# Performance work log

Measured on AMD Instinct MI355X. Metric: run time of the kernel, lower is better.

The kernel has to match this reference:

```python
import jax, jax.numpy as jnp
import numpy as np

DIM = 768      # model dim
H = 12         # heads
HD = DIM // H  # head dim = 64
T = 8          # num_frames // 2 (video temporal frames)
SF = 8         # spec_frames (audio temporal frames)
AP = 196       # audio patches per frame
VP = 196       # video patches per frame
B = 4          # batch
SCALE = HD ** (-0.5)  # 0.125


def setup_inputs() -> dict:
    key = jax.random.key(0)
    ks = jax.random.split(key, 12)
    n = lambda k, shape, s=1.0: s * jax.random.normal(k, shape, dtype=jnp.float32)
    return {
        "s_x": n(ks[0], (2 + AP, B * SF, DIM)),
        "t_x": n(ks[1], (1 + VP, B * T, DIM)),
        "clip_space_pos": n(ks[2], (AP, DIM), SCALE),
        "vmae_space_pos": n(ks[3], (VP, DIM), SCALE),
        "clip_temporal_pos": n(ks[4], (SF, DIM), SCALE),
        "vmae_temporal_pos": n(ks[5], (T, DIM), SCALE),
        "q_w": n(ks[6], (DIM, DIM), 0.02),
        "q_b": jnp.zeros((DIM,), jnp.float32),
        "kv_w": n(ks[7], (2 * DIM, DIM), 0.02),
        "kv_b": jnp.zeros((2 * DIM,), jnp.float32),
        "proj_w": n(ks[8], (DIM, DIM), 0.02),
        "proj_b": jnp.zeros((DIM,), jnp.float32),
    }


def _prep(pat, space_pos, temp_pos, tt):
    # pat: (n, b*tt, d) ; rearrange 'n (b t) d -> b t n d', add space pos,
    # 'b t n d -> b n t d', add temporal pos, 'b n t d -> b (n t) d'
    n, bt, d = pat.shape
    b = bt // tt
    x = pat.reshape(n, b, tt, d).transpose(1, 2, 0, 3)      # b t n d
    x = x + space_pos                                        # (n,d) bcast
    x = x.transpose(0, 2, 1, 3) + temp_pos                   # b n t d + (t,d)
    return x.reshape(b, n * tt, d)


def reference(s_x, t_x, clip_space_pos, vmae_space_pos, clip_temporal_pos,
              vmae_temporal_pos, q_w, q_b, kv_w, kv_b, proj_w, proj_b):
    t_x_cls = t_x[:1]                                        # (1, b*T, d)
    s_pat = _prep(s_x[2:], clip_space_pos, clip_temporal_pos, SF)   # (b, AP*SF, d)
    t_pat = _prep(t_x[1:], vmae_space_pos, vmae_temporal_pos, T)    # (b, VP*T, d)

    b, N, d = t_pat.shape
    M = s_pat.shape[1]
    q = t_pat @ q_w.T + q_b                                  # (b, N, d)
    q = q.reshape(b, N, H, HD).transpose(0, 2, 1, 3)         # b h n hd
    kv = s_pat @ kv_w.T + kv_b                               # (b, M, 2d)
    kv = kv.reshape(b, M, 2, H, HD).transpose(2, 0, 3, 1, 4) # 2 b h m hd
    k, v = kv[0], kv[1]

    attn = jax.nn.softmax(jnp.einsum('bhnd,bhmd->bhnm', q * SCALE, k), axis=-1)
    out = jnp.einsum('bhnm,bhmd->bhnd', attn, v)             # b h n hd
    out = out.transpose(0, 2, 1, 3).reshape(b, N, d)         # b n d
    out = out @ proj_w.T + proj_b

    # 'b (n t) d -> n (b t) d'
    out = out.reshape(b, VP, T, d).transpose(1, 0, 2, 3).reshape(VP, b * T, d)
    return jnp.concatenate([t_x_cls, out], axis=0)           # (1+VP, b*T, d)
```

## Files before the change

kernel.cpp:

```cpp
#include <hip/hip_runtime.h>
#include <hip/hip_bf16.h>

#define DIM 768
#define NH 12
#define HD 64
#define NSEQ 1568
#define ROWS 6272
#define QSC2 0.18033688011112042f
#define RGN 100352

typedef __attribute__((ext_vector_type(8))) short short8;
typedef __attribute__((ext_vector_type(4))) float f32x4;
typedef __attribute__((ext_vector_type(4))) unsigned short u16x4;
typedef unsigned short ushort_t;
typedef unsigned int uint_t;

static __device__ __forceinline__ ushort_t f2bf(float f) {
    union { float f; uint_t u; } c; c.f = f;
    uint_t u = c.u + 0x7fffu + ((c.u >> 16) & 1u);
    return (ushort_t)(u >> 16);
}
static __device__ __forceinline__ int cvt_pk_bf16(float lo, float hi) {
    int r;
    asm("v_cvt_pk_bf16_f32 %0, %1, %2" : "=v"(r) : "v"(lo), "v"(hi));
    return r;
}
static __device__ __forceinline__ void glds16(const short* g, short* l) {
    __builtin_amdgcn_global_load_lds(
        (const __attribute__((address_space(1))) void*)g,
        (__attribute__((address_space(3))) void*)l, 16, 0, 0);
}

#define SM_HALF(S, PF, LR)                                                    \
    {                                                                         \
        float p_[4][4];                                                       \
        _Pragma("unroll")                                                     \
        for (int jb = 0; jb < 4; ++jb) {                                      \
            _Pragma("unroll")                                                 \
            for (int r = 0; r < 4; ++r)                                       \
                p_[jb][r] = __builtin_amdgcn_exp2f(S[jb][r]);                 \
        }                                                                     \
        float rs_ = ((p_[0][0] + p_[0][1]) + (p_[0][2] + p_[0][3]))           \
                  + ((p_[1][0] + p_[1][1]) + (p_[1][2] + p_[1][3]))           \
                  + ((p_[2][0] + p_[2][1]) + (p_[2][2] + p_[2][3]))           \
                  + ((p_[3][0] + p_[3][1]) + (p_[3][2] + p_[3][3]));          \
        rs_ += __shfl_xor(rs_, 16);                                           \
        rs_ += __shfl_xor(rs_, 32);                                           \
        LR += rs_;                                                            \
        int pw_[4][2];                                                        \
        _Pragma("unroll")                                                     \
        for (int jb = 0; jb < 4; ++jb) {                                      \
            pw_[jb][0] = cvt_pk_bf16(p_[jb][0], p_[jb][1]);                   \
            pw_[jb][1] = cvt_pk_bf16(p_[jb][2], p_[jb][3]);                   \
        }                                                                     \
        _Pragma("unroll")                                                     \
        for (int jb2 = 0; jb2 < 2; ++jb2) {                                   \
            int S0_ = gh ? pw_[jb2 * 2 + 1][0] : pw_[jb2 * 2][0];             \
            int S1_ = gh ? pw_[jb2 * 2 + 1][1] : pw_[jb2 * 2][1];             \
            union { int i[4]; short8 s; } fr_;                                \
            fr_.i[0] = __builtin_amdgcn_ds_bpermute(addr0, S0_);              \
            fr_.i[1] = __builtin_amdgcn_ds_bpermute(addr0, S1_);              \
            fr_.i[2] = __builtin_amdgcn_ds_bpermute(addr1, S0_);              \
            fr_.i[3] = __builtin_amdgcn_ds_bpermute(addr1, S1_);              \
            PF[jb2] = fr_.s;                                                  \
        }                                                                     \
    }

#define PREP_HALF (ROWS * (DIM / 8))
#define W8 (DIM * DIM / 8)
#define CLS4 (32 * DIM / 4)
__global__ __launch_bounds__(256)
void prep_all(const float* __restrict__ src_t, const float* __restrict__ src_s,
              const float* __restrict__ vsp, const float* __restrict__ csp,
              const float* __restrict__ vtp, const float* __restrict__ ctp,
              const float* __restrict__ qw, const float* __restrict__ kvw,
              const float* __restrict__ pw, const float* __restrict__ txc,
              short* __restrict__ dst_t, short* __restrict__ dst_s,
              short* __restrict__ dq, short* __restrict__ dkv,
              short* __restrict__ dp, float* __restrict__ out_cls) {
    int idx = blockIdx.x * 256 + threadIdx.x;
    if (idx < 2 * PREP_HALF) {
        int sel = idx >= PREP_HALF;
        int i0  = sel ? idx - PREP_HALF : idx;
        const float* src  = sel ? src_s : src_t;
        const float* spos = sel ? csp : vsp;
        const float* tpos = sel ? ctp : vtp;
        short* dst = sel ? dst_s : dst_t;
        int d8  = i0 % (DIM / 8);
        int row = i0 / (DIM / 8);
        int b = row / NSEQ;
        int i = row % NSEQ;
        int n = i >> 3;
        int t = i & 7;
        const float4* s4 = reinterpret_cast<const float4*>(src + ((size_t)n * 32 + b * 8 + t) * DIM + d8 * 8);
        const float4* p4 = reinterpret_cast<const float4*>(spos + (size_t)n * DIM + d8 * 8);
        const float4* q4 = reinterpret_cast<const float4*>(tpos + (size_t)t * DIM + d8 * 8);
        union { int w[4]; short8 v; } o;
        float4 a0 = s4[0], a1 = s4[1], b0 = p4[0], b1 = p4[1], c0 = q4[0], c1 = q4[1];
        o.w[0] = cvt_pk_bf16(a0.x + b0.x + c0.x, a0.y + b0.y + c0.y);
        o.w[1] = cvt_pk_bf16(a0.z + b0.z + c0.z, a0.w + b0.w + c0.w);
        o.w[2] = cvt_pk_bf16(a1.x + b1.x + c1.x, a1.y + b1.y + c1.y);
        o.w[3] = cvt_pk_bf16(a1.z + b1.z + c1.z, a1.w + b1.w + c1.w);
        reinterpret_cast<short8*>(dst)[i0] = o.v;
    } else if (idx < 2 * PREP_HALF + 4 * W8) {
        int i0 = idx - 2 * PREP_HALF;
        const float* src; short* dst; int off;
        if (i0 < W8)            { src = qw;  dst = dq;  off = i0; }
        else if (i0 < 3 * W8)   { src = kvw; dst = dkv; off = i0 - W8; }
        else                    { src = pw;  dst = dp;  off = i0 - 3 * W8; }
        const float4* s4 = reinterpret_cast<const float4*>(src + (size_t)off * 8);
        float4 a0 = s4[0], a1 = s4[1];
        union { int w[4]; short8 v; } o;
        o.w[0] = cvt_pk_bf16(a0.x, a0.y);
        o.w[1] = cvt_pk_bf16(a0.z, a0.w);
        o.w[2] = cvt_pk_bf16(a1.x, a1.y);
        o.w[3] = cvt_pk_bf16(a1.z, a1.w);
        reinterpret_cast<short8*>(dst)[off] = o.v;
    } else {
        int i0 = idx - (2 * PREP_HALF + 4 * W8);
        reinterpret_cast<float4*>(out_cls)[i0] = reinterpret_cast<const float4*>(txc)[i0];
    }
}

__global__ __launch_bounds__(256)
void gemm_qkv(const short* __restrict__ tpat, const short* __restrict__ spat,
              const short* __restrict__ wq, const short* __restrict__ wkv,
              const float* __restrict__ q_b, const float* __restrict__ kv_b,
              ushort_t* __restrict__ qout, ushort_t* __restrict__ kout,
              ushort_t* __restrict__ vtout) {
    __shared__ short As[2][128 * 32];
    __shared__ short Ws[2][128 * 32];
    const int t = threadIdx.x;
    const int l = t & 63, w = t >> 6;
    const int Li = l & 15, Lg = l >> 4;
    int orig = blockIdx.x;
    int xcd = orig & 7, idxq = orig >> 3;
    int wg = (xcd < 2 ? xcd * 111 : 222 + (xcd - 2) * 110) + idxq;
    const int x = wg % 18, y = wg / 18;
    const int mode = (x >= 6);
    const short* A  = mode ? spat : tpat;
    const short* Wm = mode ? wkv : wq;
    const float* bias = mode ? kv_b : q_b;
    const int c0 = (mode ? x - 6 : x) * 128;
    const int r0 = y * 128;
    const int wrow = (w >> 1) * 64, wcol = (w & 1) * 64;

    f32x4 acc[4][4];
    #pragma unroll
    for (int i = 0; i < 4; ++i)
        #pragma unroll
        for (int j = 0; j < 4; ++j) acc[i][j] = (f32x4){0.f, 0.f, 0.f, 0.f};

    const short* Ag = A  + (size_t)(r0 + w * 32 + (l >> 2)) * DIM + (l & 3) * 8;
    const short* Wg = Wm + (size_t)(c0 + w * 32 + (l >> 2)) * DIM + (l & 3) * 8;

    glds16(Ag,                    &As[0][(w * 32) * 32]);
    glds16(Ag + (size_t)16 * DIM, &As[0][(w * 32 + 16) * 32]);
    glds16(Wg,                    &Ws[0][(w * 32) * 32]);
    glds16(Wg + (size_t)16 * DIM, &Ws[0][(w * 32 + 16) * 32]);
    __syncthreads();

    int cur = 0;
    for (int k0 = 0; k0 < DIM; k0 += 32) {
        if (k0 + 32 < DIM) {
            int nb = cur ^ 1;
            glds16(Ag + k0 + 32,                    &As[nb][(w * 32) * 32]);
            glds16(Ag + (size_t)16 * DIM + k0 + 32, &As[nb][(w * 32 + 16) * 32]);
            glds16(Wg + k0 + 32,                    &Ws[nb][(w * 32) * 32]);
            glds16(Wg + (size_t)16 * DIM + k0 + 32, &Ws[nb][(w * 32 + 16) * 32]);
        }
        short8 af[4], wf[4];
        #pragma unroll
        for (int mi = 0; mi < 4; ++mi)
            af[mi] = *reinterpret_cast<const short8*>(&As[cur][(wrow + mi * 16 + Li) * 32 + Lg * 8]);
        #pragma unroll
        for (int ni = 0; ni < 4; ++ni)
            wf[ni] = *reinterpret_cast<const short8*>(&Ws[cur][(wcol + ni * 16 + Li) * 32 + Lg * 8]);
        __builtin_amdgcn_s_setprio(1);
        #pragma unroll
        for (int mi = 0; mi < 4; ++mi)
            #pragma unroll
            for (int ni = 0; ni < 4; ++ni)
                acc[mi][ni] = __builtin_amdgcn_mfma_f32_16x16x32_bf16(af[mi], wf[ni], acc[mi][ni], 0, 0, 0);
        __builtin_amdgcn_s_setprio(0);
        __syncthreads();
        cur ^= 1;
    }

    #pragma unroll
    for (int mi = 0; mi < 4; ++mi) {
        int rowbase = r0 + wrow + mi * 16 + Lg * 4;
        int b = rowbase / NSEQ;
        int ii = rowbase - b * NSEQ;
        #pragma unroll
        for (int ni = 0; ni < 4; ++ni) {
            int c = c0 + wcol + ni * 16 + Li;
            float bv = bias[c];
            if (mode == 0) {
                int h = c >> 6, e = c & 63;
                size_t base = (size_t)(b * NH + h) * RGN + (size_t)(ii >> 4) * 1024
                            + (e >> 3) * 128 + (ii & 15) * 8 + (e & 7);
                #pragma unroll
                for (int rr = 0; rr < 4; ++rr)
                    qout[base + rr * 8] = f2bf((acc[mi][ni][rr] + bv) * QSC2);
            } else {
                if (c < DIM) {
                    int h = c >> 6, e = c & 63;
                    size_t base = (size_t)(b * NH + h) * RGN + (size_t)(ii >> 4) * 1024
                                + (e >> 3) * 128 + (ii & 15) * 8 + (e & 7);
                    #pragma unroll
                    for (int rr = 0; rr < 4; ++rr)
                        kout[base + rr * 8] = f2bf(acc[mi][ni][rr] + bv);
                } else {
                    int cc = c - DIM;
                    int h = cc >> 6, d = cc & 63;
                    size_t vbase = (size_t)(b * NH + h) * RGN + (size_t)(ii >> 5) * 2048
                                 + (d >> 4) * 512 + ((ii & 31) >> 3) * 128
                                 + (d & 15) * 8 + (ii & 7);
                    union { int w2[2]; u16x4 v; } pk;
                    pk.w2[0] = cvt_pk_bf16(acc[mi][ni][0] + bv, acc[mi][ni][1] + bv);
                    pk.w2[1] = cvt_pk_bf16(acc[mi][ni][2] + bv, acc[mi][ni][3] + bv);
                    *reinterpret_cast<u16x4*>(vtout + vbase) = pk.v;
                }
            }
        }
    }
}

__global__ __launch_bounds__(256)
void gemm_proj(const short* __restrict__ A, const short* __restrict__ Wm,
               const float* __restrict__ bias, float* __restrict__ out) {
    __shared__ short As[2][128 * 32];
    __shared__ short Ws[2][128 * 32];
    const int t = threadIdx.x;
    const int l = t & 63, w = t >> 6;
    const int Li = l & 15, Lg = l >> 4;
    int orig = blockIdx.x;
    int xcd = orig & 7, idxq = orig >> 3;
    int wg = (xcd < 6 ? xcd * 37 : 222 + (xcd - 6) * 36) + idxq;
    const int c0 = (wg % 6) * 128, r0 = (wg / 6) * 128;
    const int wrow = (w >> 1) * 64, wcol = (w & 1) * 64;

    f32x4 acc[4][4];
    #pragma unroll
    for (int i = 0; i < 4; ++i)
        #pragma unroll
        for (int j = 0; j < 4; ++j) acc[i][j] = (f32x4){0.f, 0.f, 0.f, 0.f};

    const short* Ag = A  + (size_t)(r0 + w * 32 + (l >> 2)) * DIM + (l & 3) * 8;
    const short* Wg = Wm + (size_t)(c0 + w * 32 + (l >> 2)) * DIM + (l & 3) * 8;

    glds16(Ag,                    &As[0][(w * 32) * 32]);
    glds16(Ag + (size_t)16 * DIM, &As[0][(w * 32 + 16) * 32]);
    glds16(Wg,                    &Ws[0][(w * 32) * 32]);
    glds16(Wg + (size_t)16 * DIM, &Ws[0][(w * 32 + 16) * 32]);
    __syncthreads();

    int cur = 0;
    for (int k0 = 0; k0 < DIM; k0 += 32) {
        if (k0 + 32 < DIM) {
            int nb = cur ^ 1;
            glds16(Ag + k0 + 32,                    &As[nb][(w * 32) * 32]);
            glds16(Ag + (size_t)16 * DIM + k0 + 32, &As[nb][(w * 32 + 16) * 32]);
            glds16(Wg + k0 + 32,                    &Ws[nb][(w * 32) * 32]);
            glds16(Wg + (size_t)16 * DIM + k0 + 32, &Ws[nb][(w * 32 + 16) * 32]);
        }
        short8 af[4], wf[4];
        #pragma unroll
        for (int mi = 0; mi < 4; ++mi)
            af[mi] = *reinterpret_cast<const short8*>(&As[cur][(wrow + mi * 16 + Li) * 32 + Lg * 8]);
        #pragma unroll
        for (int ni = 0; ni < 4; ++ni)
            wf[ni] = *reinterpret_cast<const short8*>(&Ws[cur][(wcol + ni * 16 + Li) * 32 + Lg * 8]);
        __builtin_amdgcn_s_setprio(1);
        #pragma unroll
        for (int mi = 0; mi < 4; ++mi)
            #pragma unroll
            for (int ni = 0; ni < 4; ++ni)
                acc[mi][ni] = __builtin_amdgcn_mfma_f32_16x16x32_bf16(af[mi], wf[ni], acc[mi][ni], 0, 0, 0);
        __builtin_amdgcn_s_setprio(0);
        __syncthreads();
        cur ^= 1;
    }

    #pragma unroll
    for (int mi = 0; mi < 4; ++mi) {
        int rowbase = r0 + wrow + mi * 16 + Lg * 4;
        int b = rowbase / NSEQ;
        int ii = rowbase - b * NSEQ;
        #pragma unroll
        for (int ni = 0; ni < 4; ++ni) {
            int c = c0 + wcol + ni * 16 + Li;
            float bv = bias[c];
            #pragma unroll
            for (int rr = 0; rr < 4; ++rr) {
                int i2 = ii + rr;
                int n = i2 >> 3, tt = i2 & 7;
                out[((size_t)(1 + n) * 32 + b * 8 + tt) * DIM + c] = acc[mi][ni][rr] + bv;
            }
        }
    }
}

__global__ __launch_bounds__(256)
void attn_bf(const short* __restrict__ qf_, const short* __restrict__ kf_,
             const short* __restrict__ vf_, ushort_t* __restrict__ ao) {
    const int t = threadIdx.x, l = t & 63, w = t >> 6;
    const int li = l & 15, g = l >> 4;
    const int bid = blockIdx.x;
    const int rest = bid >> 3;
    const int bh = (bid & 7) + 8 * (rest / 13);
    const int qx = rest % 13;
    const int b = bh / NH, h = bh % NH;
    const int q0w = qx * 128 + w * 32;
    if (q0w >= NSEQ) return;
    const size_t RB = (size_t)bh * RGN;
    const short* qR = qf_ + RB + (size_t)(q0w >> 4) * 1024 + l * 8;
    const short* kR = kf_ + RB + l * 8;
    const short* vR = vf_ + RB + l * 8;

    short8 qf0[2], qf1[2];
    qf0[0] = *reinterpret_cast<const short8*>(qR);
    qf0[1] = *reinterpret_cast<const short8*>(qR + 512);
    qf1[0] = *reinterpret_cast<const short8*>(qR + 1024);
    qf1[1] = *reinterpret_cast<const short8*>(qR + 1536);

    f32x4 o0[4], o1[4];
    #pragma unroll
    for (int i = 0; i < 4; ++i) {
        o0[i] = (f32x4){0.f, 0.f, 0.f, 0.f};
        o1[i] = (f32x4){0.f, 0.f, 0.f, 0.f};
    }
    float lr0 = 0.f, lr1 = 0.f;
    const int addr0 = (li + ((2 * g) & 3) * 16) * 4;
    const int addr1 = (li + ((2 * g + 1) & 3) * 16) * 4;
    const int gh = g >> 1;

    short8 kf[4][2];
    #pragma unroll
    for (int jb = 0; jb < 4; ++jb) {
        kf[jb][0] = *reinterpret_cast<const short8*>(kR + (size_t)jb * 1024);
        kf[jb][1] = *reinterpret_cast<const short8*>(kR + (size_t)jb * 1024 + 512);
    }

    for (int m0 = 0; m0 < NSEQ; m0 += 64) {
        short8 vf[4][2];
        {
            const short* vT = vR + (size_t)(m0 >> 5) * 2048;
            #pragma unroll
            for (int nb = 0; nb < 4; ++nb) {
                vf[nb][0] = *reinterpret_cast<const short8*>(vT + nb * 512);
                vf[nb][1] = *reinterpret_cast<const short8*>(vT + 2048 + nb * 512);
            }
        }

        f32x4 s0[4], s1[4];
        #pragma unroll
        for (int i = 0; i < 4; ++i) {
            s0[i] = (f32x4){0.f, 0.f, 0.f, 0.f};
            s1[i] = (f32x4){0.f, 0.f, 0.f, 0.f};
        }
        __builtin_amdgcn_s_setprio(1);
        #pragma unroll
        for (int jb = 0; jb < 4; ++jb) {
            s0[jb] = __builtin_amdgcn_mfma_f32_16x16x32_bf16(kf[jb][0], qf0[0], s0[jb], 0, 0, 0);
            s0[jb] = __builtin_amdgcn_mfma_f32_16x16x32_bf16(kf[jb][1], qf0[1], s0[jb], 0, 0, 0);
            s1[jb] = __builtin_amdgcn_mfma_f32_16x16x32_bf16(kf[jb][0], qf1[0], s1[jb], 0, 0, 0);
            s1[jb] = __builtin_amdgcn_mfma_f32_16x16x32_bf16(kf[jb][1], qf1[1], s1[jb], 0, 0, 0);
        }
        __builtin_amdgcn_s_setprio(0);

        if (m0 + 64 < NSEQ) {
            const short* kT = kR + (size_t)((m0 + 64) >> 4) * 1024;
            #pragma unroll
            for (int jb = 0; jb < 4; ++jb) {
                kf[jb][0] = *reinterpret_cast<const short8*>(kT + (size_t)jb * 1024);
                kf[jb][1] = *reinterpret_cast<const short8*>(kT + (size_t)jb * 1024 + 512);
            }
        }

        if (m0 + 64 > NSEQ) {
            #pragma unroll
            for (int jb = 0; jb < 4; ++jb)
                #pragma unroll
                for (int r = 0; r < 4; ++r)
                    if (m0 + jb * 16 + g * 4 + r >= NSEQ) {
                        s0[jb][r] = -1e30f;
                        s1[jb][r] = -1e30f;
                    }
        }

        short8 pf0[2], pf1[2];
        SM_HALF(s0, pf0, lr0)
        SM_HALF(s1, pf1, lr1)

        __builtin_amdgcn_s_setprio(1);
        #pragma unroll
        for (int nb = 0; nb < 4; ++nb)
            #pragma unroll
            for (int jb2 = 0; jb2 < 2; ++jb2) {
                o0[nb] = __builtin_amdgcn_mfma_f32_16x16x32_bf16(vf[nb][jb2], pf0[jb2], o0[nb], 0, 0, 0);
                o1[nb] = __builtin_amdgcn_mfma_f32_16x16x32_bf16(vf[nb][jb2], pf1[jb2], o1[nb], 0, 0, 0);
            }
        __builtin_amdgcn_s_setprio(0);
    }

    {
        float invl = 1.f / lr0;
        ushort_t* ob = ao + ((size_t)b * NSEQ + q0w + li) * DIM + h * HD;
        #pragma unroll
        for (int nb = 0; nb < 4; ++nb) {
            union { int w2[2]; u16x4 v; } pk;
            pk.w2[0] = cvt_pk_bf16(o0[nb][0] * invl, o0[nb][1] * invl);
            pk.w2[1] = cvt_pk_bf16(o0[nb][2] * invl, o0[nb][3] * invl);
            *reinterpret_cast<u16x4*>(ob + nb * 16 + g * 4) = pk.v;
        }
    }
    {
        float invl = 1.f / lr1;
        ushort_t* ob = ao + ((size_t)b * NSEQ + q0w + 16 + li) * DIM + h * HD;
        #pragma unroll
        for (int nb = 0; nb < 4; ++nb) {
            union { int w2[2]; u16x4 v; } pk;
            pk.w2[0] = cvt_pk_bf16(o1[nb][0] * invl, o1[nb][1] * invl);
            pk.w2[1] = cvt_pk_bf16(o1[nb][2] * invl, o1[nb][3] * invl);
            *reinterpret_cast<u16x4*>(ob + nb * 16 + g * 4) = pk.v;
        }
    }
}

extern "C" void kernel_launch(void* const* d_in, const int* in_sizes, int n_in,
                              void* d_out, int out_size, void* d_ws, size_t ws_size,
                              hipStream_t stream) {
    const float* s_x    = (const float*)d_in[0];
    const float* t_x    = (const float*)d_in[1];
    const float* csp    = (const float*)d_in[2];
    const float* vsp    = (const float*)d_in[3];
    const float* ctp    = (const float*)d_in[4];
    const float* vtp    = (const float*)d_in[5];
    const float* q_w    = (const float*)d_in[6];
    const float* q_b    = (const float*)d_in[7];
    const float* kv_w   = (const float*)d_in[8];
    const float* kv_b   = (const float*)d_in[9];
    const float* proj_w = (const float*)d_in[10];
    const float* proj_b = (const float*)d_in[11];
    float* out = (float*)d_out;

    const size_t S2 = (size_t)ROWS * DIM;
    const size_t SLACK = 8192;
    short* tpat = (short*)d_ws;
    short* spat = tpat + S2;
    short* qbf  = spat + S2;
    short* kbf  = qbf + S2 + SLACK;
    short* vtbf = kbf + S2 + SLACK;
    short* wq   = vtbf + S2 + SLACK;
    short* wkv  = wq + (size_t)DIM * DIM;
    short* wp   = wkv + (size_t)2 * DIM * DIM;

    prep_all<<<5880, 256, 0, stream>>>(
        t_x + (size_t)32 * DIM, s_x + (size_t)64 * DIM, vsp, csp, vtp, ctp,
        q_w, kv_w, proj_w, t_x, tpat, spat, wq, wkv, wp, out);

    gemm_qkv<<<882, 256, 0, stream>>>(tpat, spat, wq, wkv, q_b, kv_b,
                                      (ushort_t*)qbf, (ushort_t*)kbf, (ushort_t*)vtbf);
    attn_bf<<<624, 256, 0, stream>>>(qbf, kbf, vtbf, (ushort_t*)tpat);
    gemm_proj<<<294, 256, 0, stream>>>(tpat, wp, proj_b, out);
}
```

Before: 139.5 us.

## Software-pipeline attention loop and compute row sums with MFMA against ones

Restructures the attention inner loop so the PV MFMAs for the previous key block are issued alongside the QK MFMAs of the current block, with V fragments prefetched one iteration ahead and a prologue/epilogue added. The softmax row-sum reduction (adds plus cross-lane shuffles) is replaced by extra MFMAs multiplying P by a ones vector, accumulating the denominator in the matrix unit. This aims to overlap exp/permute work with matrix ops and to cut VALU and shuffle cost, at the price of more live registers and four extra MFMAs per block.

```diff
diff --git a/kernel.cpp b/kernel.cpp
--- a/kernel.cpp
+++ b/kernel.cpp
@@ -31,7 +31,7 @@
         (__attribute__((address_space(3))) void*)l, 16, 0, 0);
 }
 
-#define SM_HALF(S, PF, LR)                                                    \
+#define SM_HALF(S, PF)                                                        \
     {                                                                         \
         float p_[4][4];                                                       \
         _Pragma("unroll")                                                     \
@@ -40,13 +40,6 @@
             for (int r = 0; r < 4; ++r)                                       \
                 p_[jb][r] = __builtin_amdgcn_exp2f(S[jb][r]);                 \
         }                                                                     \
-        float rs_ = ((p_[0][0] + p_[0][1]) + (p_[0][2] + p_[0][3]))           \
-                  + ((p_[1][0] + p_[1][1]) + (p_[1][2] + p_[1][3]))           \
-                  + ((p_[2][0] + p_[2][1]) + (p_[2][2] + p_[2][3]))           \
-                  + ((p_[3][0] + p_[3][1]) + (p_[3][2] + p_[3][3]));          \
-        rs_ += __shfl_xor(rs_, 16);                                           \
-        rs_ += __shfl_xor(rs_, 32);                                           \
-        LR += rs_;                                                            \
         int pw_[4][2];                                                        \
         _Pragma("unroll")                                                     \
         for (int jb = 0; jb < 4; ++jb) {                                      \
@@ -325,35 +318,36 @@
     qf1[0] = *reinterpret_cast<const short8*>(qR + 1024);
     qf1[1] = *reinterpret_cast<const short8*>(qR + 1536);
 
+    short8 ones;
+    #pragma unroll
+    for (int i = 0; i < 8; ++i) ones[i] = (short)0x3F80;
+
     f32x4 o0[4], o1[4];
     #pragma unroll
     for (int i = 0; i < 4; ++i) {
         o0[i] = (f32x4){0.f, 0.f, 0.f, 0.f};
         o1[i] = (f32x4){0.f, 0.f, 0.f, 0.f};
     }
-    float lr0 = 0.f, lr1 = 0.f;
+    f32x4 ol0 = (f32x4){0.f, 0.f, 0.f, 0.f};
+    f32x4 ol1 = (f32x4){0.f, 0.f, 0.f, 0.f};
     const int addr0 = (li + ((2 * g) & 3) * 16) * 4;
     const int addr1 = (li + ((2 * g + 1) & 3) * 16) * 4;
     const int gh = g >> 1;
 
-    short8 kf[4][2];
+    short8 kf[4][2], vfp[4][2];
     #pragma unroll
     for (int jb = 0; jb < 4; ++jb) {
         kf[jb][0] = *reinterpret_cast<const short8*>(kR + (size_t)jb * 1024);
         kf[jb][1] = *reinterpret_cast<const short8*>(kR + (size_t)jb * 1024 + 512);
     }
-
-    for (int m0 = 0; m0 < NSEQ; m0 += 64) {
-        short8 vf[4][2];
-        {
-            const short* vT = vR + (size_t)(m0 >> 5) * 2048;
-            #pragma unroll
-            for (int nb = 0; nb < 4; ++nb) {
-                vf[nb][0] = *reinterpret_cast<const short8*>(vT + nb * 512);
-                vf[nb][1] = *reinterpret_cast<const short8*>(vT + 2048 + nb * 512);
-            }
-        }
-
+    #pragma unroll
+    for (int nb = 0; nb < 4; ++nb) {
+        vfp[nb][0] = *reinterpret_cast<const short8*>(vR + nb * 512);
+        vfp[nb][1] = *reinterpret_cast<const short8*>(vR + 2048 + nb * 512);
+    }
+
+    short8 pf0p[2], pf1p[2];
+    {
         f32x4 s0[4], s1[4];
         #pragma unroll
         for (int i = 0; i < 4; ++i) {
@@ -369,7 +363,51 @@
             s1[jb] = __builtin_amdgcn_mfma_f32_16x16x32_bf16(kf[jb][1], qf1[1], s1[jb], 0, 0, 0);
         }
         __builtin_amdgcn_s_setprio(0);
-
+        #pragma unroll
+        for (int jb = 0; jb < 4; ++jb) {
+            kf[jb][0] = *reinterpret_cast<const short8*>(kR + (size_t)(4 + jb) * 1024);
+            kf[jb][1] = *reinterpret_cast<const short8*>(kR + (size_t)(4 + jb) * 1024 + 512);
+        }
+        SM_HALF(s0, pf0p)
+        SM_HALF(s1, pf1p)
+    }
+
+    for (int m0 = 64; m0 < NSEQ; m0 += 64) {
+        f32x4 s0[4], s1[4];
+        #pragma unroll
+        for (int i = 0; i < 4; ++i) {
+            s0[i] = (f32x4){0.f, 0.f, 0.f, 0.f};
+            s1[i] = (f32x4){0.f, 0.f, 0.f, 0.f};
+        }
+        __builtin_amdgcn_s_setprio(1);
+        #pragma unroll
+        for (int jb = 0; jb < 4; ++jb) {
+            s0[jb] = __builtin_amdgcn_mfma_f32_16x16x32_bf16(kf[jb][0], qf0[0], s0[jb], 0, 0, 0);
+            s0[jb] = __builtin_amdgcn_mfma_f32_16x16x32_bf16(kf[jb][1], qf0[1], s0[jb], 0, 0, 0);
+            s1[jb] = __builtin_amdgcn_mfma_f32_16x16x32_bf16(kf[jb][0], qf1[0], s1[jb], 0, 0, 0);
+            s1[jb] = __builtin_amdgcn_mfma_f32_16x16x32_bf16(kf[jb][1], qf1[1], s1[jb], 0, 0, 0);
+        }
+        #pragma unroll
+        for (int nb = 0; nb < 4; ++nb)
+            #pragma unroll
+            for (int jb2 = 0; jb2 < 2; ++jb2) {
+                o0[nb] = __builtin_amdgcn_mfma_f32_16x16x32_bf16(vfp[nb][jb2], pf0p[jb2], o0[nb], 0, 0, 0);
+                o1[nb] = __builtin_amdgcn_mfma_f32_16x16x32_bf16(vfp[nb][jb2], pf1p[jb2], o1[nb], 0, 0, 0);
+            }
+        ol0 = __builtin_amdgcn_mfma_f32_16x16x32_bf16(ones, pf0p[0], ol0, 0, 0, 0);
+        ol0 = __builtin_amdgcn_mfma_f32_16x16x32_bf16(ones, pf0p[1], ol0, 0, 0, 0);
+        ol1 = __builtin_amdgcn_mfma_f32_16x16x32_bf16(ones, pf1p[0], ol1, 0, 0, 0);
+        ol1 = __builtin_amdgcn_mfma_f32_16x16x32_bf16(ones, pf1p[1], ol1, 0, 0, 0);
+        __builtin_amdgcn_s_setprio(0);
+
+        {
+            const short* vT = vR + (size_t)(m0 >> 5) * 2048;
+            #pragma unroll
+            for (int nb = 0; nb < 4; ++nb) {
+                vfp[nb][0] = *reinterpret_cast<const short8*>(vT + nb * 512);
+                vfp[nb][1] = *reinterpret_cast<const short8*>(vT + 2048 + nb * 512);
+            }
+        }
         if (m0 + 64 < NSEQ) {
             const short* kT = kR + (size_t)((m0 + 64) >> 4) * 1024;
             #pragma unroll
@@ -390,23 +428,26 @@
                     }
         }
 
-        short8 pf0[2], pf1[2];
-        SM_HALF(s0, pf0, lr0)
-        SM_HALF(s1, pf1, lr1)
-
-        __builtin_amdgcn_s_setprio(1);
-        #pragma unroll
-        for (int nb = 0; nb < 4; ++nb)
-            #pragma unroll
-            for (int jb2 = 0; jb2 < 2; ++jb2) {
-                o0[nb] = __builtin_amdgcn_mfma_f32_16x16x32_bf16(vf[nb][jb2], pf0[jb2], o0[nb], 0, 0, 0);
-                o1[nb] = __builtin_amdgcn_mfma_f32_16x16x32_bf16(vf[nb][jb2], pf1[jb2], o1[nb], 0, 0, 0);
-            }
-        __builtin_amdgcn_s_setprio(0);
-    }
+        SM_HALF(s0, pf0p)
+        SM_HALF(s1, pf1p)
+    }
+
+    __builtin_amdgcn_s_setprio(1);
+    #pragma unroll
+    for (int nb = 0; nb < 4; ++nb)
+        #pragma unroll
+        for (int jb2 = 0; jb2 < 2; ++jb2) {
+            o0[nb] = __builtin_amdgcn_mfma_f32_16x16x32_bf16(vfp[nb][jb2], pf0p[jb2], o0[nb], 0, 0, 0);
+            o1[nb] = __builtin_amdgcn_mfma_f32_16x16x32_bf16(vfp[nb][jb2], pf1p[jb2], o1[nb], 0, 0, 0);
+        }
+    ol0 = __builtin_amdgcn_mfma_f32_16x16x32_bf16(ones, pf0p[0], ol0, 0, 0, 0);
+    ol0 = __builtin_amdgcn_mfma_f32_16x16x32_bf16(ones, pf0p[1], ol0, 0, 0, 0);
+    ol1 = __builtin_amdgcn_mfma_f32_16x16x32_bf16(ones, pf1p[0], ol1, 0, 0, 0);
+    ol1 = __builtin_amdgcn_mfma_f32_16x16x32_bf16(ones, pf1p[1], ol1, 0, 0, 0);
+    __builtin_amdgcn_s_setprio(0);
 
     {
-        float invl = 1.f / lr0;
+        float invl = 1.f / ol0[0];
         ushort_t* ob = ao + ((size_t)b * NSEQ + q0w + li) * DIM + h * HD;
         #pragma unroll
         for (int nb = 0; nb < 4; ++nb) {
@@ -417,7 +458,7 @@
         }
     }
     {
-        float invl = 1.f / lr1;
+        float invl = 1.f / ol1[0];
         ushort_t* ob = ao + ((size_t)b * NSEQ + q0w + 16 + li) * DIM + h * HD;
         #pragma unroll
         for (int nb = 0; nb < 4; ++nb) {
```

Result: faster. 135.3 us (-3.0%).

## Software-pipeline attention K/V loads with inline asm and compute row sums via MFMA

Applied to the files above, without the earlier changes.

Rewrites the attention inner loop as a fully unrolled, double-buffered pipeline. Global K/V loads are issued through inline asm with explicit vmcnt waits and sched barriers, so the next K tile is fetched while the current tile is computed. The softmax row sum's scalar adds and cross-lane shuffles are replaced by extra MFMAs against a ones vector. It also sets a launch-bounds occupancy hint of 2 and hard-codes the tail mask for the last tile. The cost is higher register pressure and brittle manual wait counts.

```diff
diff --git a/kernel.cpp b/kernel.cpp
--- a/kernel.cpp
+++ b/kernel.cpp
@@ -31,7 +31,30 @@
         (__attribute__((address_space(3))) void*)l, 16, 0, 0);
 }
 
-#define SM_HALF(S, PF, LR)                                                    \
+#define GLOAD(dst, ptr, OFFB)                                                 \
+    asm volatile("global_load_dwordx4 %0, %1, off offset:" #OFFB              \
+                 : "=v"(dst) : "v"(ptr))
+
+#define ISSUE_K(KF, KP)                                                       \
+    { const short* kp2_ = (KP) + 2048;                                        \
+      GLOAD(KF[0][0], (KP), 0);    GLOAD(KF[0][1], (KP), 1024);               \
+      GLOAD(KF[1][0], (KP), 2048); GLOAD(KF[1][1], (KP), 3072);               \
+      GLOAD(KF[2][0], kp2_, 0);    GLOAD(KF[2][1], kp2_, 1024);               \
+      GLOAD(KF[3][0], kp2_, 2048); GLOAD(KF[3][1], kp2_, 3072); }
+
+#define ISSUE_V(VF, VP)                                                       \
+    { const short* vp2_ = (VP) + 2048;                                        \
+      GLOAD(VF[0][0], (VP), 0);    GLOAD(VF[1][0], (VP), 1024);               \
+      GLOAD(VF[2][0], (VP), 2048); GLOAD(VF[3][0], (VP), 3072);               \
+      GLOAD(VF[0][1], vp2_, 0);    GLOAD(VF[1][1], vp2_, 1024);               \
+      GLOAD(VF[2][1], vp2_, 2048); GLOAD(VF[3][1], vp2_, 3072); }
+
+#define VWAIT0 { asm volatile("s_waitcnt vmcnt(0)" ::: "memory");             \
+                 __builtin_amdgcn_sched_barrier(0); }
+#define VWAIT8 { asm volatile("s_waitcnt vmcnt(8)" ::: "memory");             \
+                 __builtin_amdgcn_sched_barrier(0); }
+
+#define SM_HALF(S, PF)                                                        \
     {                                                                         \
         float p_[4][4];                                                       \
         _Pragma("unroll")                                                     \
@@ -40,13 +63,6 @@
             for (int r = 0; r < 4; ++r)                                       \
                 p_[jb][r] = __builtin_amdgcn_exp2f(S[jb][r]);                 \
         }                                                                     \
-        float rs_ = ((p_[0][0] + p_[0][1]) + (p_[0][2] + p_[0][3]))           \
-                  + ((p_[1][0] + p_[1][1]) + (p_[1][2] + p_[1][3]))           \
-                  + ((p_[2][0] + p_[2][1]) + (p_[2][2] + p_[2][3]))           \
-                  + ((p_[3][0] + p_[3][1]) + (p_[3][2] + p_[3][3]));          \
-        rs_ += __shfl_xor(rs_, 16);                                           \
-        rs_ += __shfl_xor(rs_, 32);                                           \
-        LR += rs_;                                                            \
         int pw_[4][2];                                                        \
         _Pragma("unroll")                                                     \
         for (int jb = 0; jb < 4; ++jb) {                                      \
@@ -64,6 +80,53 @@
             fr_.i[3] = __builtin_amdgcn_ds_bpermute(addr1, S1_);              \
             PF[jb2] = fr_.s;                                                  \
         }                                                                     \
+    }
+
+#define ATT_TILE(KF, KFN, DO_ISSUEK, MASK)                                    \
+    {                                                                         \
+        VWAIT0;                                                               \
+        ISSUE_V(vf, vp); vp += 4096;                                          \
+        if (DO_ISSUEK) { ISSUE_K(KFN, kp); kp += 4096; }                      \
+        f32x4 s0_[4], s1_[4];                                                 \
+        _Pragma("unroll")                                                     \
+        for (int i_ = 0; i_ < 4; ++i_) {                                      \
+            s0_[i_] = (f32x4){0.f, 0.f, 0.f, 0.f};                            \
+            s1_[i_] = (f32x4){0.f, 0.f, 0.f, 0.f};                            \
+        }                                                                     \
+        __builtin_amdgcn_s_setprio(1);                                        \
+        _Pragma("unroll")                                                     \
+        for (int jb_ = 0; jb_ < 4; ++jb_) {                                   \
+            s0_[jb_] = __builtin_amdgcn_mfma_f32_16x16x32_bf16(KF[jb_][0], qf0[0], s0_[jb_], 0, 0, 0); \
+            s0_[jb_] = __builtin_amdgcn_mfma_f32_16x16x32_bf16(KF[jb_][1], qf0[1], s0_[jb_], 0, 0, 0); \
+            s1_[jb_] = __builtin_amdgcn_mfma_f32_16x16x32_bf16(KF[jb_][0], qf1[0], s1_[jb_], 0, 0, 0); \
+            s1_[jb_] = __builtin_amdgcn_mfma_f32_16x16x32_bf16(KF[jb_][1], qf1[1], s1_[jb_], 0, 0, 0); \
+        }                                                                     \
+        __builtin_amdgcn_s_setprio(0);                                        \
+        if (MASK) {                                                           \
+            _Pragma("unroll")                                                 \
+            for (int r_ = 0; r_ < 4; ++r_) {                                  \
+                s0_[2][r_] = -1e30f; s0_[3][r_] = -1e30f;                     \
+                s1_[2][r_] = -1e30f; s1_[3][r_] = -1e30f;                     \
+            }                                                                 \
+        }                                                                     \
+        short8 pf0_[2], pf1_[2];                                              \
+        SM_HALF(s0_, pf0_)                                                    \
+        SM_HALF(s1_, pf1_)                                                    \
+        if (DO_ISSUEK) { VWAIT8; } else { VWAIT0; }                           \
+        __builtin_amdgcn_s_setprio(1);                                        \
+        _Pragma("unroll")                                                     \
+        for (int nb_ = 0; nb_ < 4; ++nb_) {                                   \
+            _Pragma("unroll")                                                 \
+            for (int j2_ = 0; j2_ < 2; ++j2_) {                               \
+                o0[nb_] = __builtin_amdgcn_mfma_f32_16x16x32_bf16(vf[nb_][j2_], pf0_[j2_], o0[nb_], 0, 0, 0); \
+                o1[nb_] = __builtin_amdgcn_mfma_f32_16x16x32_bf16(vf[nb_][j2_], pf1_[j2_], o1[nb_], 0, 0, 0); \
+            }                                                                 \
+        }                                                                     \
+        ol0 = __builtin_amdgcn_mfma_f32_16x16x32_bf16(ones, pf0_[0], ol0, 0, 0, 0); \
+        ol0 = __builtin_amdgcn_mfma_f32_16x16x32_bf16(ones, pf0_[1], ol0, 0, 0, 0); \
+        ol1 = __builtin_amdgcn_mfma_f32_16x16x32_bf16(ones, pf1_[0], ol1, 0, 0, 0); \
+        ol1 = __builtin_amdgcn_mfma_f32_16x16x32_bf16(ones, pf1_[1], ol1, 0, 0, 0); \
+        __builtin_amdgcn_s_setprio(0);                                        \
     }
 
 #define PREP_HALF (ROWS * (DIM / 8))
@@ -302,7 +365,7 @@
     }
 }
 
-__global__ __launch_bounds__(256)
+__global__ __launch_bounds__(256, 2)
 void attn_bf(const short* __restrict__ qf_, const short* __restrict__ kf_,
              const short* __restrict__ vf_, ushort_t* __restrict__ ao) {
     const int t = threadIdx.x, l = t & 63, w = t >> 6;
@@ -316,8 +379,8 @@
     if (q0w >= NSEQ) return;
     const size_t RB = (size_t)bh * RGN;
     const short* qR = qf_ + RB + (size_t)(q0w >> 4) * 1024 + l * 8;
-    const short* kR = kf_ + RB + l * 8;
-    const short* vR = vf_ + RB + l * 8;
+    const short* kp = kf_ + RB + l * 8;
+    const short* vp = vf_ + RB + l * 8;
 
     short8 qf0[2], qf1[2];
     qf0[0] = *reinterpret_cast<const short8*>(qR);
@@ -325,88 +388,34 @@
     qf1[0] = *reinterpret_cast<const short8*>(qR + 1024);
     qf1[1] = *reinterpret_cast<const short8*>(qR + 1536);
 
+    short8 ones;
+    #pragma unroll
+    for (int i = 0; i < 8; ++i) ones[i] = (short)0x3F80;
+
     f32x4 o0[4], o1[4];
     #pragma unroll
     for (int i = 0; i < 4; ++i) {
         o0[i] = (f32x4){0.f, 0.f, 0.f, 0.f};
         o1[i] = (f32x4){0.f, 0.f, 0.f, 0.f};
     }
-    float lr0 = 0.f, lr1 = 0.f;
+    f32x4 ol0 = (f32x4){0.f, 0.f, 0.f, 0.f};
+    f32x4 ol1 = (f32x4){0.f, 0.f, 0.f, 0.f};
     const int addr0 = (li + ((2 * g) & 3) * 16) * 4;
     const int addr1 = (li + ((2 * g + 1) & 3) * 16) * 4;
     const int gh = g >> 1;
 
-    short8 kf[4][2];
-    #pragma unroll
-    for (int jb = 0; jb < 4; ++jb) {
-        kf[jb][0] = *reinterpret_cast<const short8*>(kR + (size_t)jb * 1024);
-        kf[jb][1] = *reinterpret_cast<const short8*>(kR + (size_t)jb * 1024 + 512);
-    }
-
-    for (int m0 = 0; m0 < NSEQ; m0 += 64) {
-        short8 vf[4][2];
-        {
-            const short* vT = vR + (size_t)(m0 >> 5) * 2048;
-            #pragma unroll
-            for (int nb = 0; nb < 4; ++nb) {
-                vf[nb][0] = *reinterpret_cast<const short8*>(vT + nb * 512);
-                vf[nb][1] = *reinterpret_cast<const short8*>(vT + 2048 + nb * 512);
-            }
-        }
-
-        f32x4 s0[4], s1[4];
-        #pragma unroll
-        for (int i = 0; i < 4; ++i) {
-            s0[i] = (f32x4){0.f, 0.f, 0.f, 0.f};
-            s1[i] = (f32x4){0.f, 0.f, 0.f, 0.f};
-        }
-        __builtin_amdgcn_s_setprio(1);
-        #pragma unroll
-        for (int jb = 0; jb < 4; ++jb) {
-            s0[jb] = __builtin_amdgcn_mfma_f32_16x16x32_bf16(kf[jb][0], qf0[0], s0[jb], 0, 0, 0);
-            s0[jb] = __builtin_amdgcn_mfma_f32_16x16x32_bf16(kf[jb][1], qf0[1], s0[jb], 0, 0, 0);
-            s1[jb] = __builtin_amdgcn_mfma_f32_16x16x32_bf16(kf[jb][0], qf1[0], s1[jb], 0, 0, 0);
-            s1[jb] = __builtin_amdgcn_mfma_f32_16x16x32_bf16(kf[jb][1], qf1[1], s1[jb], 0, 0, 0);
-        }
-        __builtin_amdgcn_s_setprio(0);
-
-        if (m0 + 64 < NSEQ) {
-            const short* kT = kR + (size_t)((m0 + 64) >> 4) * 1024;
-            #pragma unroll
-            for (int jb = 0; jb < 4; ++jb) {
-                kf[jb][0] = *reinterpret_cast<const short8*>(kT + (size_t)jb * 1024);
-                kf[jb][1] = *reinterpret_cast<const short8*>(kT + (size_t)jb * 1024 + 512);
-            }
-        }
-
-        if (m0 + 64 > NSEQ) {
-            #pragma unroll
-            for (int jb = 0; jb < 4; ++jb)
-                #pragma unroll
-                for (int r = 0; r < 4; ++r)
-                    if (m0 + jb * 16 + g * 4 + r >= NSEQ) {
-                        s0[jb][r] = -1e30f;
-                        s1[jb][r] = -1e30f;
-                    }
-        }
-
-        short8 pf0[2], pf1[2];
-        SM_HALF(s0, pf0, lr0)
-        SM_HALF(s1, pf1, lr1)
-
-        __builtin_amdgcn_s_setprio(1);
-        #pragma unroll
-        for (int nb = 0; nb < 4; ++nb)
-            #pragma unroll
-            for (int jb2 = 0; jb2 < 2; ++jb2) {
-                o0[nb] = __builtin_amdgcn_mfma_f32_16x16x32_bf16(vf[nb][jb2], pf0[jb2], o0[nb], 0, 0, 0);
-                o1[nb] = __builtin_amdgcn_mfma_f32_16x16x32_bf16(vf[nb][jb2], pf1[jb2], o1[nb], 0, 0, 0);
-            }
-        __builtin_amdgcn_s_setprio(0);
-    }
+    short8 kfA[4][2], kfB[4][2], vf[4][2];
+
+    ISSUE_K(kfA, kp); kp += 4096;
+
+    for (int i = 0; i < 12; ++i) {
+        ATT_TILE(kfA, kfB, true, false);
+        ATT_TILE(kfB, kfA, true, false);
+    }
+    ATT_TILE(kfA, kfB, false, true);
 
     {
-        float invl = 1.f / lr0;
+        float invl = 1.f / ol0[0];
         ushort_t* ob = ao + ((size_t)b * NSEQ + q0w + li) * DIM + h * HD;
         #pragma unroll
         for (int nb = 0; nb < 4; ++nb) {
@@ -417,7 +426,7 @@
         }
     }
     {
-        float invl = 1.f / lr1;
+        float invl = 1.f / ol1[0];
         ushort_t* ob = ao + ((size_t)b * NSEQ + q0w + 16 + li) * DIM + h * HD;
         #pragma unroll
         for (int nb = 0; nb < 4; ++nb) {
```

Measured after the change: 129.2 us (median of 2 runs). 1.08x faster.

## Stage attention K/V tiles through shared LDS and compute row sums via MFMA

Applied to the files above, without the earlier changes.

The attention kernel now cooperatively loads K/V tiles into double-buffered LDS using global_load_lds, shared by the four waves, instead of each wave reading K/V from global memory into registers. Inactive waves stay alive so they can take part in the barriers. Softmax row sums move from VALU adds and cross-lane shuffles to an extra MFMA against a vector of ones. The GEMM kernels swap __syncthreads for explicit vmcnt waits plus s_barrier so the prefetch stays in flight. This trades less global traffic and fewer VALU ops for added barrier synchronisation and LDS usage.

```diff
diff --git a/kernel.cpp b/kernel.cpp
--- a/kernel.cpp
+++ b/kernel.cpp
@@ -31,7 +31,7 @@
         (__attribute__((address_space(3))) void*)l, 16, 0, 0);
 }
 
-#define SM_HALF(S, PF, LR)                                                    \
+#define SM_HALF(S, PF)                                                        \
     {                                                                         \
         float p_[4][4];                                                       \
         _Pragma("unroll")                                                     \
@@ -40,13 +40,6 @@
             for (int r = 0; r < 4; ++r)                                       \
                 p_[jb][r] = __builtin_amdgcn_exp2f(S[jb][r]);                 \
         }                                                                     \
-        float rs_ = ((p_[0][0] + p_[0][1]) + (p_[0][2] + p_[0][3]))           \
-                  + ((p_[1][0] + p_[1][1]) + (p_[1][2] + p_[1][3]))           \
-                  + ((p_[2][0] + p_[2][1]) + (p_[2][2] + p_[2][3]))           \
-                  + ((p_[3][0] + p_[3][1]) + (p_[3][2] + p_[3][3]));          \
-        rs_ += __shfl_xor(rs_, 16);                                           \
-        rs_ += __shfl_xor(rs_, 32);                                           \
-        LR += rs_;                                                            \
         int pw_[4][2];                                                        \
         _Pragma("unroll")                                                     \
         for (int jb = 0; jb < 4; ++jb) {                                      \
@@ -158,7 +151,6 @@
     glds16(Ag + (size_t)16 * DIM, &As[0][(w * 32 + 16) * 32]);
     glds16(Wg,                    &Ws[0][(w * 32) * 32]);
     glds16(Wg + (size_t)16 * DIM, &Ws[0][(w * 32 + 16) * 32]);
-    __syncthreads();
 
     int cur = 0;
     for (int k0 = 0; k0 < DIM; k0 += 32) {
@@ -168,7 +160,12 @@
             glds16(Ag + (size_t)16 * DIM + k0 + 32, &As[nb][(w * 32 + 16) * 32]);
             glds16(Wg + k0 + 32,                    &Ws[nb][(w * 32) * 32]);
             glds16(Wg + (size_t)16 * DIM + k0 + 32, &Ws[nb][(w * 32 + 16) * 32]);
-        }
+            asm volatile("s_waitcnt vmcnt(4)" ::: "memory");
+        } else {
+            asm volatile("s_waitcnt vmcnt(0)" ::: "memory");
+        }
+        __builtin_amdgcn_sched_barrier(0);
+        __builtin_amdgcn_s_barrier();
         short8 af[4], wf[4];
         #pragma unroll
         for (int mi = 0; mi < 4; ++mi)
@@ -183,7 +180,7 @@
             for (int ni = 0; ni < 4; ++ni)
                 acc[mi][ni] = __builtin_amdgcn_mfma_f32_16x16x32_bf16(af[mi], wf[ni], acc[mi][ni], 0, 0, 0);
         __builtin_amdgcn_s_setprio(0);
-        __syncthreads();
+        __builtin_amdgcn_s_barrier();
         cur ^= 1;
     }
 
@@ -254,7 +251,6 @@
     glds16(Ag + (size_t)16 * DIM, &As[0][(w * 32 + 16) * 32]);
     glds16(Wg,                    &Ws[0][(w * 32) * 32]);
     glds16(Wg + (size_t)16 * DIM, &Ws[0][(w * 32 + 16) * 32]);
-    __syncthreads();
 
     int cur = 0;
     for (int k0 = 0; k0 < DIM; k0 += 32) {
@@ -264,7 +260,12 @@
             glds16(Ag + (size_t)16 * DIM + k0 + 32, &As[nb][(w * 32 + 16) * 32]);
             glds16(Wg + k0 + 32,                    &Ws[nb][(w * 32) * 32]);
             glds16(Wg + (size_t)16 * DIM + k0 + 32, &Ws[nb][(w * 32 + 16) * 32]);
-        }
+            asm volatile("s_waitcnt vmcnt(4)" ::: "memory");
+        } else {
+            asm volatile("s_waitcnt vmcnt(0)" ::: "memory");
+        }
+        __builtin_amdgcn_sched_barrier(0);
+        __builtin_amdgcn_s_barrier();
         short8 af[4], wf[4];
         #pragma unroll
         for (int mi = 0; mi < 4; ++mi)
@@ -279,7 +280,7 @@
             for (int ni = 0; ni < 4; ++ni)
                 acc[mi][ni] = __builtin_amdgcn_mfma_f32_16x16x32_bf16(af[mi], wf[ni], acc[mi][ni], 0, 0, 0);
         __builtin_amdgcn_s_setprio(0);
-        __syncthreads();
+        __builtin_amdgcn_s_barrier();
         cur ^= 1;
     }
 
@@ -305,6 +306,8 @@
 __global__ __launch_bounds__(256)
 void attn_bf(const short* __restrict__ qf_, const short* __restrict__ kf_,
              const short* __restrict__ vf_, ushort_t* __restrict__ ao) {
+    __shared__ short Ks[2][4096];
+    __shared__ short Vs[2][4096];
     const int t = threadIdx.x, l = t & 63, w = t >> 6;
     const int li = l & 15, g = l >> 4;
     const int bid = blockIdx.x;
@@ -313,11 +316,15 @@
     const int qx = rest % 13;
     const int b = bh / NH, h = bh % NH;
     const int q0w = qx * 128 + w * 32;
-    if (q0w >= NSEQ) return;
+    const int qrow = (q0w < NSEQ) ? q0w : 0;
     const size_t RB = (size_t)bh * RGN;
-    const short* qR = qf_ + RB + (size_t)(q0w >> 4) * 1024 + l * 8;
-    const short* kR = kf_ + RB + l * 8;
-    const short* vR = vf_ + RB + l * 8;
+    const short* qR = qf_ + RB + (size_t)(qrow >> 4) * 1024 + l * 8;
+    const short* kSrc = kf_ + RB + (size_t)(w * 2) * 512 + l * 8;
+    const short* vSrc = vf_ + RB + (size_t)(w * 2) * 512 + l * 8;
+    short* kD0a = &Ks[0][(w * 2) * 512]; short* kD0b = kD0a + 512;
+    short* kD1a = &Ks[1][(w * 2) * 512]; short* kD1b = kD1a + 512;
+    short* vD0a = &Vs[0][(w * 2) * 512]; short* vD0b = vD0a + 512;
+    short* vD1a = &Vs[1][(w * 2) * 512]; short* vD1b = vD1a + 512;
 
     short8 qf0[2], qf1[2];
     qf0[0] = *reinterpret_cast<const short8*>(qR);
@@ -325,33 +332,53 @@
     qf1[0] = *reinterpret_cast<const short8*>(qR + 1024);
     qf1[1] = *reinterpret_cast<const short8*>(qR + 1536);
 
+    short8 ones;
+    #pragma unroll
+    for (int i = 0; i < 8; ++i) ones[i] = (short)0x3F80;
+
     f32x4 o0[4], o1[4];
     #pragma unroll
     for (int i = 0; i < 4; ++i) {
         o0[i] = (f32x4){0.f, 0.f, 0.f, 0.f};
         o1[i] = (f32x4){0.f, 0.f, 0.f, 0.f};
     }
-    float lr0 = 0.f, lr1 = 0.f;
+    f32x4 ol0 = (f32x4){0.f, 0.f, 0.f, 0.f};
+    f32x4 ol1 = (f32x4){0.f, 0.f, 0.f, 0.f};
     const int addr0 = (li + ((2 * g) & 3) * 16) * 4;
     const int addr1 = (li + ((2 * g + 1) & 3) * 16) * 4;
     const int gh = g >> 1;
 
-    short8 kf[4][2];
-    #pragma unroll
-    for (int jb = 0; jb < 4; ++jb) {
-        kf[jb][0] = *reinterpret_cast<const short8*>(kR + (size_t)jb * 1024);
-        kf[jb][1] = *reinterpret_cast<const short8*>(kR + (size_t)jb * 1024 + 512);
-    }
-
-    for (int m0 = 0; m0 < NSEQ; m0 += 64) {
-        short8 vf[4][2];
-        {
-            const short* vT = vR + (size_t)(m0 >> 5) * 2048;
-            #pragma unroll
-            for (int nb = 0; nb < 4; ++nb) {
-                vf[nb][0] = *reinterpret_cast<const short8*>(vT + nb * 512);
-                vf[nb][1] = *reinterpret_cast<const short8*>(vT + 2048 + nb * 512);
-            }
+    glds16(kSrc,       kD0a);  glds16(kSrc + 512,       kD0b);
+    glds16(vSrc,       vD0a);  glds16(vSrc + 512,       vD0b);
+
+    int cur = 0;
+    for (int mt = 0; mt < 25; ++mt) {
+        if (mt < 24) {
+            size_t toff = (size_t)(mt + 1) * 4096;
+            if (cur == 0) {
+                glds16(kSrc + toff, kD1a);  glds16(kSrc + toff + 512, kD1b);
+                glds16(vSrc + toff, vD1a);  glds16(vSrc + toff + 512, vD1b);
+            } else {
+                glds16(kSrc + toff, kD0a);  glds16(kSrc + toff + 512, kD0b);
+                glds16(vSrc + toff, vD0a);  glds16(vSrc + toff + 512, vD0b);
+            }
+            asm volatile("s_waitcnt vmcnt(4)" ::: "memory");
+        } else {
+            asm volatile("s_waitcnt vmcnt(0)" ::: "memory");
+        }
+        __builtin_amdgcn_sched_barrier(0);
+        __builtin_amdgcn_s_barrier();
+
+        short8 kfr[4][2], vfr[4][2];
+        #pragma unroll
+        for (int jb = 0; jb < 4; ++jb) {
+            kfr[jb][0] = *reinterpret_cast<const short8*>(&Ks[cur][jb * 1024 + l * 8]);
+            kfr[jb][1] = *reinterpret_cast<const short8*>(&Ks[cur][jb * 1024 + 512 + l * 8]);
+        }
+        #pragma unroll
+        for (int nb = 0; nb < 4; ++nb) {
+            vfr[nb][0] = *reinterpret_cast<const short8*>(&Vs[cur][nb * 512 + l * 8]);
+            vfr[nb][1] = *reinterpret_cast<const short8*>(&Vs[cur][2048 + nb * 512 + l * 8]);
         }
 
         f32x4 s0[4], s1[4];
@@ -363,68 +390,64 @@
         __builtin_amdgcn_s_setprio(1);
         #pragma unroll
         for (int jb = 0; jb < 4; ++jb) {
-            s0[jb] = __builtin_amdgcn_mfma_f32_16x16x32_bf16(kf[jb][0], qf0[0], s0[jb], 0, 0, 0);
-            s0[jb] = __builtin_amdgcn_mfma_f32_16x16x32_bf16(kf[jb][1], qf0[1], s0[jb], 0, 0, 0);
-            s1[jb] = __builtin_amdgcn_mfma_f32_16x16x32_bf16(kf[jb][0], qf1[0], s1[jb], 0, 0, 0);
-            s1[jb] = __builtin_amdgcn_mfma_f32_16x16x32_bf16(kf[jb][1], qf1[1], s1[jb], 0, 0, 0);
+            s0[jb] = __builtin_amdgcn_mfma_f32_16x16x32_bf16(kfr[jb][0], qf0[0], s0[jb], 0, 0, 0);
+            s0[jb] = __builtin_amdgcn_mfma_f32_16x16x32_bf16(kfr[jb][1], qf0[1], s0[jb], 0, 0, 0);
+            s1[jb] = __builtin_amdgcn_mfma_f32_16x16x32_bf16(kfr[jb][0], qf1[0], s1[jb], 0, 0, 0);
+            s1[jb] = __builtin_amdgcn_mfma_f32_16x16x32_bf16(kfr[jb][1], qf1[1], s1[jb], 0, 0, 0);
         }
         __builtin_amdgcn_s_setprio(0);
-
-        if (m0 + 64 < NSEQ) {
-            const short* kT = kR + (size_t)((m0 + 64) >> 4) * 1024;
-            #pragma unroll
-            for (int jb = 0; jb < 4; ++jb) {
-                kf[jb][0] = *reinterpret_cast<const short8*>(kT + (size_t)jb * 1024);
-                kf[jb][1] = *reinterpret_cast<const short8*>(kT + (size_t)jb * 1024 + 512);
-            }
-        }
-
-        if (m0 + 64 > NSEQ) {
-            #pragma unroll
-            for (int jb = 0; jb < 4; ++jb)
-                #pragma unroll
-                for (int r = 0; r < 4; ++r)
-                    if (m0 + jb * 16 + g * 4 + r >= NSEQ) {
-                        s0[jb][r] = -1e30f;
-                        s1[jb][r] = -1e30f;
-                    }
+        if (mt == 24) {
+            #pragma unroll
+            for (int r = 0; r < 4; ++r) {
+                s0[2][r] = -1e30f; s0[3][r] = -1e30f;
+                s1[2][r] = -1e30f; s1[3][r] = -1e30f;
+            }
         }
 
         short8 pf0[2], pf1[2];
-        SM_HALF(s0, pf0, lr0)
-        SM_HALF(s1, pf1, lr1)
+        SM_HALF(s0, pf0)
+        SM_HALF(s1, pf1)
 
         __builtin_amdgcn_s_setprio(1);
         #pragma unroll
         for (int nb = 0; nb < 4; ++nb)
             #pragma unroll
-            for (int jb2 = 0; jb2 < 2; ++jb2) {
-                o0[nb] = __builtin_amdgcn_mfma_f32_16x16x32_bf16(vf[nb][jb2], pf0[jb2], o0[nb], 0, 0, 0);
-                o1[nb] = __builtin_amdgcn_mfma_f32_16x16x32_bf16(vf[nb][jb2], pf1[jb2], o1[nb], 0, 0, 0);
-            }
+            for (int j2 = 0; j2 < 2; ++j2) {
+                o0[nb] = __builtin_amdgcn_mfma_f32_16x16x32_bf16(vfr[nb][j2], pf0[j2], o0[nb], 0, 0, 0);
+                o1[nb] = __builtin_amdgcn_mfma_f32_16x16x32_bf16(vfr[nb][j2], pf1[j2], o1[nb], 0, 0, 0);
+            }
+        ol0 = __builtin_amdgcn_mfma_f32_16x16x32_bf16(ones, pf0[0], ol0, 0, 0, 0);
+        ol0 = __builtin_amdgcn_mfma_f32_16x16x32_bf16(ones, pf0[1], ol0, 0, 0, 0);
+        ol1 = __builtin_amdgcn_mfma_f32_16x16x32_bf16(ones, pf1[0], ol1, 0, 0, 0);
+        ol1 = __builtin_amdgcn_mfma_f32_16x16x32_bf16(ones, pf1[1], ol1, 0, 0, 0);
         __builtin_amdgcn_s_setprio(0);
-    }
-
-    {
-        float invl = 1.f / lr0;
-        ushort_t* ob = ao + ((size_t)b * NSEQ + q0w + li) * DIM + h * HD;
-        #pragma unroll
-        for (int nb = 0; nb < 4; ++nb) {
-            union { int w2[2]; u16x4 v; } pk;
-            pk.w2[0] = cvt_pk_bf16(o0[nb][0] * invl, o0[nb][1] * invl);
-            pk.w2[1] = cvt_pk_bf16(o0[nb][2] * invl, o0[nb][3] * invl);
-            *reinterpret_cast<u16x4*>(ob + nb * 16 + g * 4) = pk.v;
-        }
-    }
-    {
-        float invl = 1.f / lr1;
-        ushort_t* ob = ao + ((size_t)b * NSEQ + q0w + 16 + li) * DIM + h * HD;
-        #pragma unroll
-        for (int nb = 0; nb < 4; ++nb) {
-            union { int w2[2]; u16x4 v; } pk;
-            pk.w2[0] = cvt_pk_bf16(o1[nb][0] * invl, o1[nb][1] * invl);
-            pk.w2[1] = cvt_pk_bf16(o1[nb][2] * invl, o1[nb][3] * invl);
-            *reinterpret_cast<u16x4*>(ob + nb * 16 + g * 4) = pk.v;
+
+        __builtin_amdgcn_s_barrier();
+        cur ^= 1;
+    }
+
+    if (q0w < NSEQ) {
+        {
+            float invl = 1.f / ol0[0];
+            ushort_t* ob = ao + ((size_t)b * NSEQ + q0w + li) * DIM + h * HD;
+            #pragma unroll
+            for (int nb = 0; nb < 4; ++nb) {
+                union { int w2[2]; u16x4 v; } pk;
+                pk.w2[0] = cvt_pk_bf16(o0[nb][0] * invl, o0[nb][1] * invl);
+                pk.w2[1] = cvt_pk_bf16(o0[nb][2] * invl, o0[nb][3] * invl);
+                *reinterpret_cast<u16x4*>(ob + nb * 16 + g * 4) = pk.v;
+            }
+        }
+        {
+            float invl = 1.f / ol1[0];
+            ushort_t* ob = ao + ((size_t)b * NSEQ + q0w + 16 + li) * DIM + h * HD;
+            #pragma unroll
+            for (int nb = 0; nb < 4; ++nb) {
+                union { int w2[2]; u16x4 v; } pk;
+                pk.w2[0] = cvt_pk_bf16(o1[nb][0] * invl, o1[nb][1] * invl);
+                pk.w2[1] = cvt_pk_bf16(o1[nb][2] * invl, o1[nb][3] * invl);
+                *reinterpret_cast<u16x4*>(ob + nb * 16 + g * 4) = pk.v;
+            }
         }
     }
 }
```

After: 148.6 us. +6.5%, slower.
